# Performance work log

Hardware: AMD Instinct MI355X
Metric: run time of the kernel (lower is better)

## Reference

```python
import jax, jax.numpy as jnp
import numpy as np

B, T, C = 2, 2048, 2048
H, KVH, HD = 16, 4, 128  # heads, kv heads, head_dim
G = H // KVH             # GQA group size
THETA = 10000.0


def _rope_cos_sin(t, hd, dtype):
    inv_freq = 1.0 / (THETA ** (jnp.arange(0, hd, 2, dtype=jnp.float32) / hd))
    pos = jnp.arange(t, dtype=jnp.float32)
    freqs = pos[:, None] * inv_freq[None, :]          # [T, hd/2]
    emb = jnp.concatenate([freqs, freqs], axis=-1)    # [T, hd]
    return jnp.cos(emb).astype(dtype), jnp.sin(emb).astype(dtype)


def _rotate_half(x):
    x1, x2 = jnp.split(x, 2, axis=-1)
    return jnp.concatenate([-x2, x1], axis=-1)


def setup_inputs() -> dict:
    key = jax.random.key(0)
    ks = jax.random.split(key, 5)
    s_in = 1.0 / np.sqrt(C)
    return {
        "x": jax.random.normal(ks[0], (B, T, C), jnp.float32),
        "wq": jax.random.normal(ks[1], (C, H * HD), jnp.float32) * s_in,
        "bq": jnp.zeros((H * HD,), jnp.float32),
        "wk": jax.random.normal(ks[2], (C, KVH * HD), jnp.float32) * s_in,
        "bk": jnp.zeros((KVH * HD,), jnp.float32),
        "wv": jax.random.normal(ks[3], (C, KVH * HD), jnp.float32) * s_in,
        "bv": jnp.zeros((KVH * HD,), jnp.float32),
        "wo": jax.random.normal(ks[4], (H * HD, C), jnp.float32) * (1.0 / np.sqrt(H * HD)),
    }


def reference(x, wq, bq, wk, bk, wv, bv, wo):
    b, t, c = x.shape
    q = (x @ wq + bq).reshape(b, t, H, HD).transpose(0, 2, 1, 3)    # [B,H,T,hd]
    k = (x @ wk + bk).reshape(b, t, KVH, HD).transpose(0, 2, 1, 3)  # [B,KVH,T,hd]
    v = (x @ wv + bv).reshape(b, t, KVH, HD).transpose(0, 2, 1, 3)

    cos, sin = _rope_cos_sin(t, HD, x.dtype)  # [T,hd]
    q = q * cos + _rotate_half(q) * sin
    k = k * cos + _rotate_half(k) * sin

    # GQA: group query heads over kv heads
    qg = q.reshape(b, KVH, G, t, HD)
    scale = 1.0 / np.sqrt(HD)
    scores = jnp.einsum('bkgtd,bksd->bkgts', qg, k) * scale  # [B,KVH,G,T,T]
    causal = jnp.tril(jnp.ones((t, t), bool))
    scores = jnp.where(causal, scores, jnp.finfo(scores.dtype).min)
    attn = jax.nn.softmax(scores, axis=-1)
    out = jnp.einsum('bkgts,bksd->bkgtd', attn, v)            # [B,KVH,G,T,hd]
    out = out.reshape(b, H, t, HD).transpose(0, 2, 1, 3).reshape(b, t, H * HD)
    return out @ wo
```

## Files before the change

kernel.cpp:

```cpp
#include <hip/hip_runtime.h>
#include <hip/hip_bf16.h>
#include <math.h>

#define B_ 2
#define T_ 2048
#define C_ 2048
#define H_ 16
#define KVH_ 4
#define HD_ 128
#define G_ (H_ / KVH_)
#define MROWS (B_ * T_)
#define NQKV (H_ * HD_ + 2 * KVH_ * HD_)
#define KOFF (H_ * HD_)
#define VOFF (H_ * HD_ + KVH_ * HD_)
#define L2T (13.287712379549449f / 64.0f)

typedef __hip_bfloat16 bf16;
typedef short bf16x8 __attribute__((ext_vector_type(8)));
typedef short bf16x4 __attribute__((ext_vector_type(4)));
typedef float f32x4 __attribute__((ext_vector_type(4)));

__device__ __forceinline__ void gload_lds16(const void* g, void* l) {
  __builtin_amdgcn_global_load_lds(
      (const __attribute__((address_space(1))) unsigned int*)g,
      (__attribute__((address_space(3))) unsigned int*)l, 16, 0, 0);
}

static __device__ __forceinline__ f32x4 mfma32k(bf16x8 a, bf16x8 b, f32x4 c) {
  return __builtin_amdgcn_mfma_f32_16x16x32_bf16(a, b, c, 0, 0, 0);
}

static __device__ __forceinline__ short f2bf(float x) {
  unsigned u = __builtin_bit_cast(unsigned, x);
  u += 0x7FFFu + ((u >> 16) & 1u);
  return (short)(u >> 16);
}

static __device__ __forceinline__ float bfh2f(short h) {
  unsigned u = ((unsigned)(unsigned short)h) << 16;
  return __builtin_bit_cast(float, u);
}

static __device__ __forceinline__ float fexp2(float x) {
#if __has_builtin(__builtin_amdgcn_exp2f)
  return __builtin_amdgcn_exp2f(x);
#else
  return exp2f(x);
#endif
}

__global__ __launch_bounds__(256) void prep_kernel(
    const float* __restrict__ x, bf16* __restrict__ xb,
    const float* __restrict__ wq, const float* __restrict__ wk,
    const float* __restrict__ wv, bf16* __restrict__ wqkvT,
    const float* __restrict__ wo, bf16* __restrict__ woT,
    float2* __restrict__ tab) {
  __shared__ float t[32][33];
  int bid = blockIdx.x;
  if (bid < 8192) {
    const int i = (bid * 256 + threadIdx.x) * 4;
    float4 v = *(const float4*)(x + i);
    xb[i + 0] = __float2bfloat16(v.x);
    xb[i + 1] = __float2bfloat16(v.y);
    xb[i + 2] = __float2bfloat16(v.z);
    xb[i + 3] = __float2bfloat16(v.w);
    return;
  }
  bid -= 8192;
  if (bid < 6144) {
    const int tx = threadIdx.x & 31, ty = threadIdx.x >> 5;
    const int c0 = (bid % 96) * 32;
    const int r0 = (bid / 96) * 32;
    const float* src;
    int nn, ld;
    if (c0 < KOFF)      { src = wq; nn = c0;        ld = 2048; }
    else if (c0 < VOFF) { src = wk; nn = c0 - KOFF; ld = 512; }
    else                { src = wv; nn = c0 - VOFF; ld = 512; }
#pragma unroll
    for (int it = 0; it < 4; ++it)
      t[ty + 8 * it][tx] = src[(size_t)(r0 + ty + 8 * it) * ld + nn + tx];
    __syncthreads();
#pragma unroll
    for (int it = 0; it < 4; ++it)
      wqkvT[(size_t)(c0 + ty + 8 * it) * 2048 + r0 + tx] =
          __float2bfloat16(t[tx][ty + 8 * it]);
    return;
  }
  bid -= 6144;
  if (bid < 4096) {
    const int tx = threadIdx.x & 31, ty = threadIdx.x >> 5;
    const int c0 = (bid & 63) * 32;
    const int r0 = (bid >> 6) * 32;
#pragma unroll
    for (int it = 0; it < 4; ++it)
      t[ty + 8 * it][tx] = wo[(size_t)(r0 + ty + 8 * it) * 2048 + c0 + tx];
    __syncthreads();
#pragma unroll
    for (int it = 0; it < 4; ++it)
      woT[(size_t)(c0 + ty + 8 * it) * 2048 + r0 + tx] =
          __float2bfloat16(t[tx][ty + 8 * it]);
    return;
  }
  bid -= 4096;
  {
    const int idx = bid * 256 + threadIdx.x;
    const int tt = idx >> 6, i = idx & 63;
    const float invf = fexp2(-(float)i * L2T);
    float s, c;
    __sincosf((float)tt * invf, &s, &c);
    tab[idx] = make_float2(c, s);
  }
}

__global__ __launch_bounds__(256) void pack_kv(const bf16* __restrict__ qkv,
                                               bf16* __restrict__ kp,
                                               bf16* __restrict__ vp,
                                               const float2* __restrict__ tab) {
  const int pid = blockIdx.x;
  if (pid < 512) {
    const int tile = pid & 63;
    const int bk = pid >> 6;
    const int b = bk >> 2, kvh = bk & 3;
#pragma unroll
    for (int u = 0; u < 2; ++u) {
      const int t = threadIdx.x + u * 256;
      const int kc = t >> 6, L = t & 63;
      const int trow = tile * 32 + ((L >> 2) & 3) * 8 + (kc >> 2) * 4 + (L & 3);
      const bf16* src = qkv + (size_t)(b * T_ + trow) * NQKV +
                        KOFF + kvh * HD_ + (kc & 3) * 32 + (L >> 4) * 8;
      bf16x8 vs = *(const bf16x8*)src;
      bf16x8 vpair = *(const bf16x8*)(src + (((kc & 2) == 0) ? 64 : -64));
      const float2* tp = tab + trow * 64 + (kc & 1) * 32 + (L >> 4) * 8;
      bf16x8 outv;
#pragma unroll
      for (int jj = 0; jj < 8; ++jj) {
        const float2 cs = tp[jj];
        const float a = bfh2f(vs[jj]), p = bfh2f(vpair[jj]);
        outv[jj] = f2bf(((kc & 2) == 0) ? (a * cs.x - p * cs.y)
                                        : (a * cs.x + p * cs.y));
      }
      *(bf16x8*)(kp + ((size_t)(bk * 64 + tile) * 8 + kc) * 512 + L * 8) = outv;
    }
    return;
  }
  {
    const int pid2 = pid - 512;
    const int tile = pid2 & 63;
    const int bk = pid2 >> 6;
    const int b = bk >> 2, kvh = bk & 3;
#pragma unroll
    for (int u = 0; u < 2; ++u) {
      const int t = threadIdx.x + u * 256;
      const int ht = t >> 6, L = t & 63;
      const int colL = L & 15, quad = L >> 4;
      const bf16* base = qkv + (size_t)(b * T_ + tile * 32 + quad * 8) * NQKV +
                         VOFF + kvh * HD_ + ht * 16 + colL;
      bf16x8 v;
#pragma unroll
      for (int jj = 0; jj < 8; ++jj)
        v[jj] = *(const short*)(base + (size_t)jj * NQKV);
      *(bf16x8*)(vp + ((size_t)(bk * 64 + tile) * 8 + ht) * 512 + L * 8) = v;
    }
  }
}

template <bool BF16OUT>
__global__ __launch_bounds__(256, 2) void gemm_mfma(
    const bf16* __restrict__ A, const bf16* __restrict__ Bt, void* __restrict__ Cout,
    const float* __restrict__ bq, const float* __restrict__ bk2,
    const float* __restrict__ bv2, int M, int N, int K) {
  __shared__ __align__(16) bf16 As[128 * 32];
  __shared__ __align__(16) bf16 Bs[128 * 32];
  const int tid = threadIdx.x;
  const int w = tid >> 6, lane = tid & 63;
  const int colL = lane & 15, quad = lane >> 4;
  const int wm = w & 1, wn = w >> 1;
  const int r0 = blockIdx.y * 128, c0 = blockIdx.x * 128;

  f32x4 acc[4][4];
  const f32x4 zero = {0.f, 0.f, 0.f, 0.f};
#pragma unroll
  for (int mt = 0; mt < 4; ++mt)
#pragma unroll
    for (int nt = 0; nt < 4; ++nt) acc[mt][nt] = zero;

  for (int k0 = 0; k0 < K; k0 += 32) {
    __syncthreads();
#pragma unroll
    for (int it = 0; it < 2; ++it) {
      const int seg = it * 4 + w;
      const int idx = seg * 64 + lane;
      const int row = idx >> 2, off = idx & 3;
      gload_lds16(A + (size_t)(r0 + row) * K + k0 + off * 8, &As[seg * 512]);
      gload_lds16(Bt + (size_t)(c0 + row) * K + k0 + off * 8, &Bs[seg * 512]);
    }
    __syncthreads();
    bf16x8 af[4], bfv[4];
#pragma unroll
    for (int mt = 0; mt < 4; ++mt)
      af[mt] = *(const bf16x8*)&As[(wm * 64 + mt * 16 + colL) * 32 + quad * 8];
#pragma unroll
    for (int nt = 0; nt < 4; ++nt)
      bfv[nt] = *(const bf16x8*)&Bs[(wn * 64 + nt * 16 + colL) * 32 + quad * 8];
#pragma unroll
    for (int mt = 0; mt < 4; ++mt)
#pragma unroll
      for (int nt = 0; nt < 4; ++nt)
        acc[mt][nt] =
            __builtin_amdgcn_mfma_f32_16x16x32_bf16(af[mt], bfv[nt], acc[mt][nt], 0, 0, 0);
  }

#pragma unroll
  for (int nt = 0; nt < 4; ++nt) {
    const int c = c0 + wn * 64 + nt * 16 + colL;
    float bias = 0.f;
    if (bq) bias = (c < KOFF) ? bq[c] : (c < VOFF ? bk2[c - KOFF] : bv2[c - VOFF]);
#pragma unroll
    for (int mt = 0; mt < 4; ++mt) {
#pragma unroll
      for (int i = 0; i < 4; ++i) {
        const int r = r0 + wm * 64 + mt * 16 + quad * 4 + i;
        const float v = acc[mt][nt][i] + bias;
        if (BF16OUT)
          ((bf16*)Cout)[(size_t)r * N + c] = __float2bfloat16(v);
        else
          ((float*)Cout)[(size_t)r * N + c] = v;
      }
    }
  }
}

__global__ __launch_bounds__(512, 1) void gemm_qkv8(
    const bf16* __restrict__ A, const bf16* __restrict__ Bt, bf16* __restrict__ Cout,
    const float* __restrict__ bq, const float* __restrict__ bk2,
    const float* __restrict__ bv2, int M, int N, int K) {
  __shared__ __align__(16) bf16 As[2][256 * 64];
  __shared__ __align__(16) bf16 Bs[2][256 * 64];
  const int tid = threadIdx.x;
  const int w = tid >> 6, lane = tid & 63;
  const int colL = lane & 15, quad = lane >> 4;
  const int wm = w >> 2, wn = w & 3;
  const int r0 = blockIdx.y * 256, c0 = blockIdx.x * 256;
  const int c7 = colL & 7;
  const int sl0 = (quad ^ c7) * 8;
  const int sl1 = ((quad + 4) ^ c7) * 8;
  const int lrow = lane >> 3;
  const int lsl = ((lane & 7) ^ lrow) * 8;
  const int nk = K >> 6;

  const bf16* pa = A + (size_t)(r0 + w * 8 + lrow) * K + lsl;
  const bf16* pb = Bt + (size_t)(c0 + w * 8 + lrow) * K + lsl;

  auto stA = [&](int kt, int bi, int q) {
    gload_lds16(pa + (size_t)q * 64 * K + kt * 64, &As[bi][(q * 64 + w * 8) * 64]);
  };
  auto stB = [&](int kt, int bi, int q) {
    gload_lds16(pb + (size_t)q * 64 * K + kt * 64, &Bs[bi][(q * 64 + w * 8) * 64]);
  };

  f32x4 acc[8][4];
  const f32x4 zero = {0.f, 0.f, 0.f, 0.f};
#pragma unroll
  for (int m = 0; m < 8; ++m)
#pragma unroll
    for (int n = 0; n < 4; ++n) acc[m][n] = zero;

  stA(0, 0, 0); stA(0, 0, 2);
  stB(0, 0, 0); stB(0, 0, 1); stB(0, 0, 2); stB(0, 0, 3);
  stA(0, 0, 1); stA(0, 0, 3);
  asm volatile("s_waitcnt vmcnt(2)" ::: "memory");
  __builtin_amdgcn_s_barrier();

#pragma unroll 1
  for (int t = 0; t < nk; ++t) {
    const int bi = t & 1, nb = bi ^ 1;
    const bool st = (t + 1 < nk);
    const bf16* Ab = &As[bi][(wm * 128 + colL) * 64];
    const bf16* Bb = &Bs[bi][(wn * 64 + colL) * 64];
    bf16x8 afr[4], bfr[4];

#pragma unroll
    for (int m = 0; m < 4; ++m) afr[m] = *(const bf16x8*)(Ab + m * 16 * 64 + sl0);
#pragma unroll
    for (int n = 0; n < 4; ++n) bfr[n] = *(const bf16x8*)(Bb + n * 16 * 64 + sl0);
    if (st) { stA(t + 1, nb, 0); stA(t + 1, nb, 2); }
    __builtin_amdgcn_s_barrier();
    __builtin_amdgcn_s_setprio(1);
#pragma unroll
    for (int m = 0; m < 4; ++m)
#pragma unroll
      for (int n = 0; n < 4; ++n) acc[m][n] = mfma32k(afr[m], bfr[n], acc[m][n]);
    __builtin_amdgcn_s_setprio(0);
    if (st) asm volatile("s_waitcnt vmcnt(2)" ::: "memory");
    else    asm volatile("s_waitcnt vmcnt(0)" ::: "memory");
    __builtin_amdgcn_s_barrier();

#pragma unroll
    for (int m = 0; m < 4; ++m)
      afr[m] = *(const bf16x8*)(Ab + (64 + m * 16) * 64 + sl0);
    if (st) { stB(t + 1, nb, 0); stB(t + 1, nb, 1); }
    __builtin_amdgcn_s_barrier();
    __builtin_amdgcn_s_setprio(1);
#pragma unroll
    for (int m = 0; m < 4; ++m)
#pragma unroll
      for (int n = 0; n < 4; ++n) acc[m + 4][n] = mfma32k(afr[m], bfr[n], acc[m + 4][n]);
    __builtin_amdgcn_s_setprio(0);
    __builtin_amdgcn_s_barrier();

#pragma unroll
    for (int m = 0; m < 4; ++m) afr[m] = *(const bf16x8*)(Ab + m * 16 * 64 + sl1);
#pragma unroll
    for (int n = 0; n < 4; ++n) bfr[n] = *(const bf16x8*)(Bb + n * 16 * 64 + sl1);
    if (st) { stB(t + 1, nb, 2); stB(t + 1, nb, 3); }
    __builtin_amdgcn_s_barrier();
    __builtin_amdgcn_s_setprio(1);
#pragma unroll
    for (int m = 0; m < 4; ++m)
#pragma unroll
      for (int n = 0; n < 4; ++n) acc[m][n] = mfma32k(afr[m], bfr[n], acc[m][n]);
    __builtin_amdgcn_s_setprio(0);
    __builtin_amdgcn_s_barrier();

#pragma unroll
    for (int m = 0; m < 4; ++m)
      afr[m] = *(const bf16x8*)(Ab + (64 + m * 16) * 64 + sl1);
    if (st) { stA(t + 1, nb, 1); stA(t + 1, nb, 3); }
    __builtin_amdgcn_s_barrier();
    __builtin_amdgcn_s_setprio(1);
#pragma unroll
    for (int m = 0; m < 4; ++m)
#pragma unroll
      for (int n = 0; n < 4; ++n) acc[m + 4][n] = mfma32k(afr[m], bfr[n], acc[m + 4][n]);
    __builtin_amdgcn_s_setprio(0);
    if (st) asm volatile("s_waitcnt vmcnt(2)" ::: "memory");
    __builtin_amdgcn_s_barrier();
  }

#pragma unroll
  for (int nt = 0; nt < 4; ++nt) {
    const int c = c0 + wn * 64 + nt * 16 + colL;
    const float bias = (c < KOFF) ? bq[c] : (c < VOFF ? bk2[c - KOFF] : bv2[c - VOFF]);
#pragma unroll
    for (int mt = 0; mt < 8; ++mt) {
#pragma unroll
      for (int i = 0; i < 4; ++i) {
        const int r = r0 + wm * 128 + mt * 16 + quad * 4 + i;
        Cout[(size_t)r * N + c] = __float2bfloat16(acc[mt][nt][i] + bias);
      }
    }
  }
}

#define FA_SCL2 (0.08838834764831845f * 1.4426950408889634f)
#define FA_M2 16.0f

__global__ __launch_bounds__(256, 3) void flash_mfma8(
    const bf16* __restrict__ qkv, const bf16* __restrict__ kp,
    const bf16* __restrict__ vp, bf16* __restrict__ ao,
    const float2* __restrict__ tab) {
  __shared__ __align__(16) bf16 KS[3][4096];
  __shared__ __align__(16) bf16 VS[3][4096];

  const int id = blockIdx.x;
  const int bk = id & 7;
  const int u = id >> 3;
  const int jq = 127 - u;
  const int b = bk >> 2, kvh = bk & 3;
  const int w = threadIdx.x >> 6;
  const int h = (kvh << 2) | w;
  const int lane = threadIdx.x & 63;
  const int colL = lane & 15, quad = lane >> 4;
  const int myq0 = jq * 16;
  const int nkv = (jq >> 1) + 1;

  const bf16* kpt = kp + ((size_t)(bk * 64)) * 4096 + (w * 2) * 512 + lane * 8;
  const bf16* vpt = vp + ((size_t)(bk * 64)) * 4096 + (w * 2) * 512 + lane * 8;

  auto stageK = [&](int tile, int slot) {
    const bf16* s = kpt + (size_t)tile * 4096;
    bf16* d = &KS[slot][(w * 2) * 512];
    gload_lds16(s, d);
    gload_lds16(s + 512, d + 512);
  };
  auto stageV = [&](int tile, int slot) {
    const bf16* s = vpt + (size_t)tile * 4096;
    bf16* d = &VS[slot][(w * 2) * 512];
    gload_lds16(s, d);
    gload_lds16(s + 512, d + 512);
  };

  bf16x8 qf[4];
  {
    const bf16* qg = qkv + (size_t)(b * T_ + myq0) * NQKV + h * HD_;
    bf16x8 rq[4];
#pragma unroll
    for (int c = 0; c < 4; ++c)
      rq[c] = *(const bf16x8*)(qg + (size_t)colL * NQKV + c * 32 + quad * 8);
    const float2* tp = tab + (myq0 + colL) * 64 + quad * 8;
    float2 cs0[8], cs1[8];
#pragma unroll
    for (int jj = 0; jj < 8; ++jj) { cs0[jj] = tp[jj]; cs1[jj] = tp[32 + jj]; }
#pragma unroll
    for (int c = 0; c < 4; ++c) {
#pragma unroll
      for (int jj = 0; jj < 8; ++jj) {
        const float2 cs = (c & 1) ? cs1[jj] : cs0[jj];
        const float a = bfh2f(rq[c][jj]), p = bfh2f(rq[c ^ 2][jj]);
        qf[c][jj] = f2bf((c & 2) ? (a * cs.x + p * cs.y)
                                 : (a * cs.x - p * cs.y));
      }
    }
  }

  const f32x4 zero = {0.f, 0.f, 0.f, 0.f};
  auto qk = [&](const bf16* Kb, f32x4 (&s_)[2]) {
    s_[0] = zero; s_[1] = zero;
#pragma unroll
    for (int c = 0; c < 4; ++c) {
      bf16x8 kf0 = *(const bf16x8*)(Kb + c * 512 + lane * 8);
      bf16x8 kf1 = *(const bf16x8*)(Kb + (4 + c) * 512 + lane * 8);
      s_[0] = mfma32k(kf0, qf[c], s_[0]);
      s_[1] = mfma32k(kf1, qf[c], s_[1]);
    }
  };

  f32x4 o[8];
#pragma unroll
  for (int ht = 0; ht < 8; ++ht) o[ht] = zero;
  float l_ = 0.f;

  stageK(0, 0);
  if (nkv > 1) stageK(1, 1);
  if (nkv > 2) stageK(2, 2);
  stageV(0, 0);
  if (nkv > 1) stageV(1, 1);
  asm volatile("s_waitcnt vmcnt(0)\n\ts_barrier" ::: "memory");

  f32x4 sA[2], sB[2];
  qk(KS[0], sA);

  int kStage = 0, kNext = 1, vRead = 0, vStage = 2;
#pragma unroll 1
  for (int tt = 0; tt < nkv; ++tt) {
    const bool sk = (tt + 3 < nkv), sv = (tt + 2 < nkv);
    if (sk) stageK(tt + 3, kStage);
    if (sv) stageV(tt + 2, vStage);

    if (tt + 1 < nkv) qk(KS[kNext], sB);

    bf16x4 pf[2];
    if (tt == nkv - 1) {
      const int qg = ((jq & 1) << 4) | colL;
#pragma unroll
      for (int kt = 0; kt < 2; ++kt) {
        const int kb = quad * 8 + kt * 4;
        float pv[4];
#pragma unroll
        for (int i = 0; i < 4; ++i) {
          float e = fexp2(fmaf(sA[kt][i], FA_SCL2, -FA_M2));
          pv[i] = (kb + i <= qg) ? e : 0.f;
        }
        l_ += (pv[0] + pv[1]) + (pv[2] + pv[3]);
        pf[kt] = (bf16x4){f2bf(pv[0]), f2bf(pv[1]), f2bf(pv[2]), f2bf(pv[3])};
      }
    } else {
#pragma unroll
      for (int kt = 0; kt < 2; ++kt) {
        float pv[4];
#pragma unroll
        for (int i = 0; i < 4; ++i)
          pv[i] = fexp2(fmaf(sA[kt][i], FA_SCL2, -FA_M2));
        l_ += (pv[0] + pv[1]) + (pv[2] + pv[3]);
        pf[kt] = (bf16x4){f2bf(pv[0]), f2bf(pv[1]), f2bf(pv[2]), f2bf(pv[3])};
      }
    }

    {
      const bf16* Vb = VS[vRead];
      const bf16x8 pcat = __builtin_shufflevector(pf[0], pf[1], 0, 1, 2, 3, 4, 5, 6, 7);
#pragma unroll
      for (int ht = 0; ht < 8; ++ht) {
        bf16x8 vf8 = *(const bf16x8*)(Vb + ht * 512 + lane * 8);
        o[ht] = mfma32k(vf8, pcat, o[ht]);
      }
    }

    if (sk)      asm volatile("s_waitcnt vmcnt(4)\n\ts_barrier" ::: "memory");
    else if (sv) asm volatile("s_waitcnt vmcnt(2)\n\ts_barrier" ::: "memory");
    else         asm volatile("s_waitcnt vmcnt(0)\n\ts_barrier" ::: "memory");

    sA[0] = sB[0]; sA[1] = sB[1];
    kStage = (kStage == 2) ? 0 : kStage + 1;
    kNext  = (kNext == 2) ? 0 : kNext + 1;
    vRead  = (vRead == 2) ? 0 : vRead + 1;
    vStage = (vStage == 2) ? 0 : vStage + 1;
  }

  {
    float lv = l_;
    lv += __shfl_xor(lv, 16);
    lv += __shfl_xor(lv, 32);
    const float rl = 1.f / lv;
    const size_t rbase = (size_t)(b * T_ + myq0 + colL) * (H_ * HD_) + h * HD_;
#pragma unroll
    for (int ht = 0; ht < 8; ++ht) {
      bf16x4 ov;
#pragma unroll
      for (int i = 0; i < 4; ++i) ov[i] = f2bf(o[ht][i] * rl);
      *(bf16x4*)(ao + rbase + ht * 16 + quad * 4) = ov;
    }
  }
}

extern "C" void kernel_launch(void* const* d_in, const int* in_sizes, int n_in,
                              void* d_out, int out_size, void* d_ws, size_t ws_size,
                              hipStream_t stream) {
  (void)in_sizes; (void)n_in; (void)out_size; (void)ws_size;
  const float* x  = (const float*)d_in[0];
  const float* wq = (const float*)d_in[1];
  const float* bq = (const float*)d_in[2];
  const float* wk = (const float*)d_in[3];
  const float* bk = (const float*)d_in[4];
  const float* wv = (const float*)d_in[5];
  const float* bv = (const float*)d_in[6];
  const float* wo = (const float*)d_in[7];
  float* out = (float*)d_out;

  char* ws = (char*)d_ws;
  bf16* xb    = (bf16*)ws;
  bf16* wqkvT = (bf16*)(ws + (16u << 20));
  bf16* woT   = (bf16*)(ws + (28u << 20));
  bf16* qkv   = (bf16*)(ws + (36u << 20));
  bf16* kp    = (bf16*)(ws + (60u << 20));
  bf16* vp    = (bf16*)(ws + (68u << 20));
  float2* tab = (float2*)(ws + (76u << 20));

  prep_kernel<<<dim3(18944), dim3(256), 0, stream>>>(
      x, xb, wq, wk, wv, wqkvT, wo, woT, tab);

  gemm_qkv8<<<dim3(NQKV / 256, MROWS / 256), dim3(512), 0, stream>>>(
      xb, wqkvT, qkv, bq, bk, bv, MROWS, NQKV, C_);

  pack_kv<<<dim3(1024), dim3(256), 0, stream>>>(qkv, kp, vp, tab);

  bf16* ao = xb;
  flash_mfma8<<<dim3(1024), dim3(256), 0, stream>>>(qkv, kp, vp, ao, tab);

  gemm_mfma<false><<<dim3(C_ / 128, MROWS / 128), dim3(256), 0, stream>>>(
      ao, woT, out, nullptr, nullptr, nullptr, MROWS, C_, KOFF);
}
```

Baseline: 311.5 us.

## Generalize 8-wave GEMM over N-tile width and use it for QKV and output projections

Templates the 8-wave double-buffered GEMM on the number of N fragments per wave. The QKV projection now uses 256x192 tiles (a 16x16 grid of 256 blocks) and the output projection uses 256x128 tiles in place of the simpler 128x128 single-buffered kernel. The aim is a grid that matches the CU count and better pipelining and LDS reuse for the output GEMM. In exchange, each wave does fewer MFMAs per LDS load, and the reordered B/A staging schedule must still line up with the vmcnt waits.

```diff
diff --git a/kernel.cpp b/kernel.cpp
--- a/kernel.cpp
+++ b/kernel.cpp
@@ -164,83 +164,19 @@
   }
 }
 
-template <bool BF16OUT>
-__global__ __launch_bounds__(256, 2) void gemm_mfma(
+template <int NF, bool BF16OUT>
+__global__ __launch_bounds__(512, 1) void gemm8(
     const bf16* __restrict__ A, const bf16* __restrict__ Bt, void* __restrict__ Cout,
     const float* __restrict__ bq, const float* __restrict__ bk2,
     const float* __restrict__ bv2, int M, int N, int K) {
-  __shared__ __align__(16) bf16 As[128 * 32];
-  __shared__ __align__(16) bf16 Bs[128 * 32];
-  const int tid = threadIdx.x;
-  const int w = tid >> 6, lane = tid & 63;
-  const int colL = lane & 15, quad = lane >> 4;
-  const int wm = w & 1, wn = w >> 1;
-  const int r0 = blockIdx.y * 128, c0 = blockIdx.x * 128;
-
-  f32x4 acc[4][4];
-  const f32x4 zero = {0.f, 0.f, 0.f, 0.f};
-#pragma unroll
-  for (int mt = 0; mt < 4; ++mt)
-#pragma unroll
-    for (int nt = 0; nt < 4; ++nt) acc[mt][nt] = zero;
-
-  for (int k0 = 0; k0 < K; k0 += 32) {
-    __syncthreads();
-#pragma unroll
-    for (int it = 0; it < 2; ++it) {
-      const int seg = it * 4 + w;
-      const int idx = seg * 64 + lane;
-      const int row = idx >> 2, off = idx & 3;
-      gload_lds16(A + (size_t)(r0 + row) * K + k0 + off * 8, &As[seg * 512]);
-      gload_lds16(Bt + (size_t)(c0 + row) * K + k0 + off * 8, &Bs[seg * 512]);
-    }
-    __syncthreads();
-    bf16x8 af[4], bfv[4];
-#pragma unroll
-    for (int mt = 0; mt < 4; ++mt)
-      af[mt] = *(const bf16x8*)&As[(wm * 64 + mt * 16 + colL) * 32 + quad * 8];
-#pragma unroll
-    for (int nt = 0; nt < 4; ++nt)
-      bfv[nt] = *(const bf16x8*)&Bs[(wn * 64 + nt * 16 + colL) * 32 + quad * 8];
-#pragma unroll
-    for (int mt = 0; mt < 4; ++mt)
-#pragma unroll
-      for (int nt = 0; nt < 4; ++nt)
-        acc[mt][nt] =
-            __builtin_amdgcn_mfma_f32_16x16x32_bf16(af[mt], bfv[nt], acc[mt][nt], 0, 0, 0);
-  }
-
-#pragma unroll
-  for (int nt = 0; nt < 4; ++nt) {
-    const int c = c0 + wn * 64 + nt * 16 + colL;
-    float bias = 0.f;
-    if (bq) bias = (c < KOFF) ? bq[c] : (c < VOFF ? bk2[c - KOFF] : bv2[c - VOFF]);
-#pragma unroll
-    for (int mt = 0; mt < 4; ++mt) {
-#pragma unroll
-      for (int i = 0; i < 4; ++i) {
-        const int r = r0 + wm * 64 + mt * 16 + quad * 4 + i;
-        const float v = acc[mt][nt][i] + bias;
-        if (BF16OUT)
-          ((bf16*)Cout)[(size_t)r * N + c] = __float2bfloat16(v);
-        else
-          ((float*)Cout)[(size_t)r * N + c] = v;
-      }
-    }
-  }
-}
-
-__global__ __launch_bounds__(512, 1) void gemm_qkv8(
-    const bf16* __restrict__ A, const bf16* __restrict__ Bt, bf16* __restrict__ Cout,
-    const float* __restrict__ bq, const float* __restrict__ bk2,
-    const float* __restrict__ bv2, int M, int N, int K) {
+  constexpr int BN = NF * 64;
   __shared__ __align__(16) bf16 As[2][256 * 64];
-  __shared__ __align__(16) bf16 Bs[2][256 * 64];
+  __shared__ __align__(16) bf16 Bs[2][BN * 64];
   const int tid = threadIdx.x;
   const int w = tid >> 6, lane = tid & 63;
   const int colL = lane & 15, quad = lane >> 4;
   const int wm = w >> 2, wn = w & 3;
-  const int r0 = blockIdx.y * 256, c0 = blockIdx.x * 256;
+  const int r0 = blockIdx.y * 256, c0 = blockIdx.x * BN;
   const int c7 = colL & 7;
   const int sl0 = (quad ^ c7) * 8;
   const int sl1 = ((quad + 4) ^ c7) * 8;
@@ -258,15 +194,16 @@
     gload_lds16(pb + (size_t)q * 64 * K + kt * 64, &Bs[bi][(q * 64 + w * 8) * 64]);
   };
 
-  f32x4 acc[8][4];
+  f32x4 acc[8][NF];
   const f32x4 zero = {0.f, 0.f, 0.f, 0.f};
 #pragma unroll
   for (int m = 0; m < 8; ++m)
 #pragma unroll
-    for (int n = 0; n < 4; ++n) acc[m][n] = zero;
+    for (int n = 0; n < NF; ++n) acc[m][n] = zero;
 
   stA(0, 0, 0); stA(0, 0, 2);
-  stB(0, 0, 0); stB(0, 0, 1); stB(0, 0, 2); stB(0, 0, 3);
+  stB(0, 0, 0); stB(0, 0, 1);
+  if constexpr (NF == 3) stB(0, 0, 2);
   stA(0, 0, 1); stA(0, 0, 3);
   asm volatile("s_waitcnt vmcnt(2)" ::: "memory");
   __builtin_amdgcn_s_barrier();
@@ -276,20 +213,20 @@
     const int bi = t & 1, nb = bi ^ 1;
     const bool st = (t + 1 < nk);
     const bf16* Ab = &As[bi][(wm * 128 + colL) * 64];
-    const bf16* Bb = &Bs[bi][(wn * 64 + colL) * 64];
-    bf16x8 afr[4], bfr[4];
+    const bf16* Bb = &Bs[bi][(wn * (NF * 16) + colL) * 64];
+    bf16x8 afr[4], bfr[NF];
 
 #pragma unroll
     for (int m = 0; m < 4; ++m) afr[m] = *(const bf16x8*)(Ab + m * 16 * 64 + sl0);
 #pragma unroll
-    for (int n = 0; n < 4; ++n) bfr[n] = *(const bf16x8*)(Bb + n * 16 * 64 + sl0);
+    for (int n = 0; n < NF; ++n) bfr[n] = *(const bf16x8*)(Bb + n * 16 * 64 + sl0);
     if (st) { stA(t + 1, nb, 0); stA(t + 1, nb, 2); }
     __builtin_amdgcn_s_barrier();
     __builtin_amdgcn_s_setprio(1);
 #pragma unroll
     for (int m = 0; m < 4; ++m)
 #pragma unroll
-      for (int n = 0; n < 4; ++n) acc[m][n] = mfma32k(afr[m], bfr[n], acc[m][n]);
+      for (int n = 0; n < NF; ++n) acc[m][n] = mfma32k(afr[m], bfr[n], acc[m][n]);
     __builtin_amdgcn_s_setprio(0);
     if (st) asm volatile("s_waitcnt vmcnt(2)" ::: "memory");
     else    asm volatile("s_waitcnt vmcnt(0)" ::: "memory");
@@ -304,49 +241,57 @@
 #pragma unroll
     for (int m = 0; m < 4; ++m)
 #pragma unroll
-      for (int n = 0; n < 4; ++n) acc[m + 4][n] = mfma32k(afr[m], bfr[n], acc[m + 4][n]);
+      for (int n = 0; n < NF; ++n) acc[m + 4][n] = mfma32k(afr[m], bfr[n], acc[m + 4][n]);
     __builtin_amdgcn_s_setprio(0);
     __builtin_amdgcn_s_barrier();
 
 #pragma unroll
     for (int m = 0; m < 4; ++m) afr[m] = *(const bf16x8*)(Ab + m * 16 * 64 + sl1);
 #pragma unroll
-    for (int n = 0; n < 4; ++n) bfr[n] = *(const bf16x8*)(Bb + n * 16 * 64 + sl1);
-    if (st) { stB(t + 1, nb, 2); stB(t + 1, nb, 3); }
+    for (int n = 0; n < NF; ++n) bfr[n] = *(const bf16x8*)(Bb + n * 16 * 64 + sl1);
+    if (st) {
+      if constexpr (NF == 3) stB(t + 1, nb, 2);
+      stA(t + 1, nb, 1);
+    }
     __builtin_amdgcn_s_barrier();
     __builtin_amdgcn_s_setprio(1);
 #pragma unroll
     for (int m = 0; m < 4; ++m)
 #pragma unroll
-      for (int n = 0; n < 4; ++n) acc[m][n] = mfma32k(afr[m], bfr[n], acc[m][n]);
+      for (int n = 0; n < NF; ++n) acc[m][n] = mfma32k(afr[m], bfr[n], acc[m][n]);
     __builtin_amdgcn_s_setprio(0);
     __builtin_amdgcn_s_barrier();
 
 #pragma unroll
     for (int m = 0; m < 4; ++m)
       afr[m] = *(const bf16x8*)(Ab + (64 + m * 16) * 64 + sl1);
-    if (st) { stA(t + 1, nb, 1); stA(t + 1, nb, 3); }
+    if (st) stA(t + 1, nb, 3);
     __builtin_amdgcn_s_barrier();
     __builtin_amdgcn_s_setprio(1);
 #pragma unroll
     for (int m = 0; m < 4; ++m)
 #pragma unroll
-      for (int n = 0; n < 4; ++n) acc[m + 4][n] = mfma32k(afr[m], bfr[n], acc[m + 4][n]);
+      for (int n = 0; n < NF; ++n) acc[m + 4][n] = mfma32k(afr[m], bfr[n], acc[m + 4][n]);
     __builtin_amdgcn_s_setprio(0);
     if (st) asm volatile("s_waitcnt vmcnt(2)" ::: "memory");
     __builtin_amdgcn_s_barrier();
   }
 
 #pragma unroll
-  for (int nt = 0; nt < 4; ++nt) {
-    const int c = c0 + wn * 64 + nt * 16 + colL;
-    const float bias = (c < KOFF) ? bq[c] : (c < VOFF ? bk2[c - KOFF] : bv2[c - VOFF]);
+  for (int nt = 0; nt < NF; ++nt) {
+    const int c = c0 + wn * (NF * 16) + nt * 16 + colL;
+    float bias = 0.f;
+    if (bq) bias = (c < KOFF) ? bq[c] : (c < VOFF ? bk2[c - KOFF] : bv2[c - VOFF]);
 #pragma unroll
     for (int mt = 0; mt < 8; ++mt) {
 #pragma unroll
       for (int i = 0; i < 4; ++i) {
         const int r = r0 + wm * 128 + mt * 16 + quad * 4 + i;
-        Cout[(size_t)r * N + c] = __float2bfloat16(acc[mt][nt][i] + bias);
+        const float v = acc[mt][nt][i] + bias;
+        if (BF16OUT)
+          ((bf16*)Cout)[(size_t)r * N + c] = __float2bfloat16(v);
+        else
+          ((float*)Cout)[(size_t)r * N + c] = v;
       }
     }
   }
@@ -539,7 +484,7 @@
   prep_kernel<<<dim3(18944), dim3(256), 0, stream>>>(
       x, xb, wq, wk, wv, wqkvT, wo, woT, tab);
 
-  gemm_qkv8<<<dim3(NQKV / 256, MROWS / 256), dim3(512), 0, stream>>>(
+  gemm8<3, true><<<dim3(16, 16), dim3(512), 0, stream>>>(
       xb, wqkvT, qkv, bq, bk, bv, MROWS, NQKV, C_);
 
   pack_kv<<<dim3(1024), dim3(256), 0, stream>>>(qkv, kp, vp, tab);
@@ -547,6 +492,6 @@
   bf16* ao = xb;
   flash_mfma8<<<dim3(1024), dim3(256), 0, stream>>>(qkv, kp, vp, ao, tab);
 
-  gemm_mfma<false><<<dim3(C_ / 128, MROWS / 128), dim3(256), 0, stream>>>(
+  gemm8<2, false><<<dim3(16, 16), dim3(512), 0, stream>>>(
       ao, woT, out, nullptr, nullptr, nullptr, MROWS, C_, KOFF);
 }
```

After: 311.1 us. Within noise of the previous version (-0.1%).
